# Performance work log

Hardware: AMD Instinct MI355X
Metric: run time of the kernel (lower is better)

The kernel has to match this reference:

```python
import jax, jax.numpy as jnp
import numpy as np

B, CIN, COUT, WID, M1, M2, H, W = 8, 3, 3, 16, 8, 8, 256, 256


def _fftfreq(n, d):
    # torch.fft.fftfreq(n, d); d may be a traced scalar
    k = np.concatenate([np.arange(0, (n - 1) // 2 + 1), np.arange(-(n // 2), 0)]).astype(np.float32)
    return jnp.asarray(k) / (n * d)


def _cplx(ri):
    return jax.lax.complex(ri[..., 0], ri[..., 1])


def _inorm(v, eps=1e-5):
    # InstanceNorm2d, affine=False: normalize over spatial dims per (b, c)
    mu = jnp.mean(v, axis=(-2, -1), keepdims=True)
    var = jnp.var(v, axis=(-2, -1), keepdims=True)
    return (v - mu) * jax.lax.rsqrt(var + eps)


def setup_inputs() -> dict:
    key = jax.random.key(0)
    ks = jax.random.split(key, 13)
    scale = 1.0 / (WID * WID)
    u = lambda k, s: scale * (0.5 + 0.5 * jax.random.uniform(k, s, jnp.float32))
    return {
        "x": jax.random.normal(ks[0], (B, CIN, H, W), jnp.float32),
        "fc0_w": jax.random.normal(ks[1], (CIN + 2, WID), jnp.float32) * 0.1,
        "fc0_b": jax.random.normal(ks[2], (WID,), jnp.float32) * 0.01,
        "pole1_ri": u(ks[3], (WID, WID, M1, 2)),
        "pole2_ri": u(ks[4], (WID, WID, M2, 2)),
        "residue_ri": u(ks[5], (WID, WID, M1, M2, 2)),
        "w0_w": jax.random.normal(ks[6], (WID, WID), jnp.float32) * 0.1,
        "w0_b": jax.random.normal(ks[7], (WID,), jnp.float32) * 0.01,
        "fc1_w": jax.random.normal(ks[8], (WID, 128), jnp.float32) * 0.1,
        "fc1_b": jax.random.normal(ks[9], (128,), jnp.float32) * 0.01,
        "fc2_w": jax.random.normal(ks[10], (128, COUT), jnp.float32) * 0.1,
        "fc2_b": jax.random.normal(ks[11], (COUT,), jnp.float32) * 0.01,
        "tx": jnp.linspace(0.0, 1.0, W, dtype=jnp.float32).reshape(1, W),
        "ty": jnp.linspace(0.0, 1.0, H, dtype=jnp.float32).reshape(1, H),
    }


def _pr2d(v, p1, p2, res, tx, ty):
    # v: [b, i, h, w] real; p1:[i,k,m1], p2:[i,k,m2], res:[i,k,m1,m2] complex
    b, i, h, w = v.shape
    dty = ty[0, 1] - ty[0, 0]
    dtx = tx[0, 1] - tx[0, 0]
    alpha = jnp.fft.fft2(v)  # [b,i,h,w] complex64
    lam1 = (2j * jnp.pi) * _fftfreq(h, dty)  # [h]
    lam2 = (2j * jnp.pi) * _fftfreq(w, dtx)  # [w]
    A1 = 1.0 / (lam1[None, None, None, :] - p1[..., None])  # [i,k,p,h]
    A2 = 1.0 / (lam2[None, None, None, :] - p2[..., None])  # [i,k,q,w]
    # output_residue1[b,k,o,x] = sum_{i,p,q} alpha[b,i,o,x] res[i,k,p,q] A1[i,k,p,o] A2[i,k,q,x]
    T = jnp.einsum('ikpq,ikpo->ikqo', res, A1)
    G = jnp.einsum('ikqo,ikqx->ikox', T, A2)        # [i,k,h,w] pole-residue transfer kernel
    out1 = jnp.einsum('biox,ikox->bkox', alpha, G)
    x1 = jnp.fft.ifft2(out1).real
    # output_residue2[b,k,p,q] = sum_{i,o,x} alpha[b,i,o,x] res[i,k,p,q] A1[i,k,p,o] A2[i,k,q,x]
    S = jnp.einsum('biox,ikqx->bikoq', alpha, A2)
    Mt = jnp.einsum('bikoq,ikpo->bikpq', S, A1)
    out2 = jnp.einsum('bikpq,ikpq->bkpq', Mt, res)  # [b,k,m1,m2]
    # transient part: x2[n,i,z,x] = sum_{b,p,q} out2[n,b,p,q] exp(p1[b,i,p] ty[z]) exp(p2[b,i,q] tx[x])
    tyc = ty.reshape(-1).astype(p1.dtype)
    txc = tx.reshape(-1).astype(p2.dtype)
    E1 = jnp.exp(p1[..., None] * tyc)  # [i,k,p,h]
    E2 = jnp.exp(p2[..., None] * txc)  # [i,k,q,w]
    U = jnp.einsum('nbpq,bipz->nbiqz', out2, E1)
    x2 = jnp.einsum('nbiqz,biqx->nizx', U, E2).real / (w * h)
    return x1 + x2


def reference(x, fc0_w, fc0_b, pole1_ri, pole2_ri, residue_ri, w0_w, w0_b,
              fc1_w, fc1_b, fc2_w, fc2_b, tx, ty):
    b, c, h, w = x.shape
    v = jnp.transpose(x, (0, 2, 3, 1))  # [b,h,w,c]
    gx = jnp.broadcast_to(jnp.linspace(0.0, 1.0, h, dtype=x.dtype)[None, :, None, None], (b, h, w, 1))
    gy = jnp.broadcast_to(jnp.linspace(0.0, 1.0, w, dtype=x.dtype)[None, None, :, None], (b, h, w, 1))
    v = jnp.concatenate([v, gx, gy], axis=-1)
    v = v @ fc0_w + fc0_b                 # [b,h,w,width]
    v = jnp.transpose(v, (0, 3, 1, 2))    # [b,width,h,w]
    p1, p2, res = _cplx(pole1_ri), _cplx(pole2_ri), _cplx(residue_ri)
    x1 = _inorm(_pr2d(_inorm(v), p1, p2, res, tx, ty))
    x2 = jnp.einsum('bihw,oi->bohw', v, w0_w) + w0_b[None, :, None, None]  # 1x1 conv
    u = x1 + x2
    u = jnp.transpose(u, (0, 2, 3, 1))
    u = jnp.sin(u @ fc1_w + fc1_b)
    u = u @ fc2_w + fc2_b
    return jnp.transpose(u, (0, 3, 1, 2))
```

## Files before the change

### kernel.cpp

```cpp
#include <hip/hip_runtime.h>
#include <cstddef>

#define NPIX 65536
#define PI_F 3.14159265358979323846f

__device__ __forceinline__ void cacc(float2& acc, float2 a, float2 b) {
  acc.x = fmaf(a.x, b.x, fmaf(-a.y, b.y, acc.x));
  acc.y = fmaf(a.x, b.y, fmaf(a.y, b.x, acc.y));
}

__device__ __forceinline__ void fft256_wave(float* re, float* im,
    const float* twr, const float* twi, int lane) {
  #pragma unroll
  for (int s = 0; s < 8; ++s) {
    __builtin_amdgcn_wave_barrier();
    const int half = 1 << s;
    #pragma unroll
    for (int r = 0; r < 2; ++r) {
      int m  = lane + 64*r;
      int t  = m & (half - 1);
      int g  = m >> s;
      int i0 = (g << (s+1)) + t;
      int i1 = i0 + half;
      int ti = t << (7 - s);
      float wr = twr[ti], wi = twi[ti];
      float br = re[i1], bi = im[i1];
      float vr = br*wr - bi*wi;
      float vi = br*wi + bi*wr;
      float ar = re[i0], ai = im[i0];
      re[i0] = ar + vr; im[i0] = ai + vi;
      re[i1] = ar - vr; im[i1] = ai - vi;
    }
  }
  __builtin_amdgcn_wave_barrier();
}

__global__ __launch_bounds__(256) void k_setup(const float2* __restrict__ p1,
    const float2* __restrict__ p2, const float* __restrict__ txv,
    const float* __restrict__ tyv, float2* __restrict__ A1,
    float2* __restrict__ A2T, float2* __restrict__ A2L,
    float2* __restrict__ E1, float2* __restrict__ E2) {
  int gid = blockIdx.x*256 + threadIdx.x;
  int o = gid & 255, p = (gid>>8)&7, k = (gid>>11)&15, i = gid>>15;
  float ko = (o < 128) ? (float)o : (float)(o - 256);
  float dty = tyv[1] - tyv[0];
  float dtx = txv[1] - txv[0];
  const float TWO_PI = 6.283185307179586f;
  {
    float lam = TWO_PI * ko / (256.0f * dty);
    float2 pv = p1[(i*16+k)*8 + p];
    float xr = -pv.x, yi = lam - pv.y;
    float D = xr*xr + yi*yi;
    A1[((size_t)((i*16+k)*8 + p))*256 + o] = make_float2(xr/D, -yi/D);
    float tv = tyv[o];
    float m = expf(pv.x*tv);
    E1[((size_t)((i*16+k)*8 + p))*256 + o] = make_float2(m*cosf(pv.y*tv), m*sinf(pv.y*tv));
  }
  {
    float lam = TWO_PI * ko / (256.0f * dtx);
    float2 pv = p2[(i*16+k)*8 + p];
    float xr = -pv.x, yi = lam - pv.y;
    float D = xr*xr + yi*yi;
    float2 val = make_float2(xr/D, -yi/D);
    A2T[((size_t)i*256 + o)*128 + k*8 + p] = val;
    A2L[((size_t)((i*16+k)*8 + p))*256 + o] = val;
    float tv = txv[o];
    float m = expf(pv.x*tv);
    E2[((size_t)((i*16+k)*8 + p))*256 + o] = make_float2(m*cosf(pv.y*tv), m*sinf(pv.y*tv));
  }
}

__global__ __launch_bounds__(256) void k_T(const float2* __restrict__ res,
    const float2* __restrict__ A1, float2* __restrict__ Tt) {
  int ik = blockIdx.x, tid = threadIdx.x;
  __shared__ float2 rbuf[64];
  __shared__ float2 a1[8][256];
  if (tid < 64) rbuf[tid] = res[(size_t)ik*64 + tid];
  for (int e = 0; e < 8; ++e) {
    int lin = tid + 256*e;
    int p = lin >> 8, o = lin & 255;
    a1[p][o] = A1[((size_t)ik*8 + p)*256 + o];
  }
  __syncthreads();
  int o = tid;
  #pragma unroll
  for (int q = 0; q < 8; ++q) {
    float2 acc = make_float2(0.f, 0.f);
    #pragma unroll
    for (int p = 0; p < 8; ++p) cacc(acc, rbuf[p*8+q], a1[p][o]);
    Tt[((size_t)ik*8 + q)*256 + o] = acc;
  }
}

__global__ __launch_bounds__(256) void k_stats_v(const float* __restrict__ x,
    const float* __restrict__ fc0w, const float* __restrict__ fc0b,
    float2* __restrict__ stats) {
  int img = blockIdx.x, tid = threadIdx.x;
  int k = img & 15, b = img >> 4;
  float w0 = fc0w[k], w1 = fc0w[16+k], w2 = fc0w[32+k], w3 = fc0w[48+k], w4 = fc0w[64+k];
  float base = fc0b[k] + (tid*(1.0f/255.0f))*w4;
  const float* xb = x + (size_t)b*3*NPIX;
  float s = 0.f, s2 = 0.f;
  for (int it = 0; it < 256; ++it) {
    int p = it*256 + tid;
    float val = base + (it*(1.0f/255.0f))*w3 + xb[p]*w0 + xb[NPIX+p]*w1 + xb[2*NPIX+p]*w2;
    s += val; s2 += val*val;
  }
  __shared__ float rs[256], rq[256];
  rs[tid] = s; rq[tid] = s2;
  __syncthreads();
  for (int off = 128; off > 0; off >>= 1) {
    if (tid < off) { rs[tid] += rs[tid+off]; rq[tid] += rq[tid+off]; }
    __syncthreads();
  }
  if (tid == 0) {
    float mean = rs[0] * (1.0f/65536.0f);
    float var  = rq[0] * (1.0f/65536.0f) - mean*mean;
    stats[img] = make_float2(mean, rsqrtf(var + 1e-5f));
  }
}

__global__ __launch_bounds__(256) void k_stats_p(const float* __restrict__ v,
    float2* __restrict__ stats) {
  int img = blockIdx.x, tid = threadIdx.x;
  const float* p = v + (size_t)img*NPIX;
  float s = 0.f, s2 = 0.f;
  for (int it = 0; it < 256; ++it) { float a = p[it*256 + tid]; s += a; s2 += a*a; }
  __shared__ float rs[256], rq[256];
  rs[tid] = s; rq[tid] = s2;
  __syncthreads();
  for (int off = 128; off > 0; off >>= 1) {
    if (tid < off) { rs[tid] += rs[tid+off]; rq[tid] += rq[tid+off]; }
    __syncthreads();
  }
  if (tid == 0) {
    float mean = rs[0] * (1.0f/65536.0f);
    float var  = rq[0] * (1.0f/65536.0f) - mean*mean;
    stats[img] = make_float2(mean, rsqrtf(var + 1e-5f));
  }
}

__global__ __launch_bounds__(256) void k_fft_v(const float* __restrict__ x,
    const float* __restrict__ fc0w, const float* __restrict__ fc0b,
    const float2* __restrict__ stats, float2* __restrict__ out) {
  __shared__ float sre[4][256], sim[4][256];
  __shared__ float twr[128], twi[128];
  int tid = threadIdx.x, lane = tid & 63, rowi = tid >> 6;
  int bid = blockIdx.x;
  int img = bid >> 6;
  int h   = (bid & 63)*4 + rowi;
  int k = img & 15, b = img >> 4;
  if (tid < 128) {
    float ang = (PI_F/128.0f)*tid;
    twr[tid] = cosf(ang); twi[tid] = -sinf(ang);
  }
  float2 st = stats[img];
  float w0 = fc0w[k], w1 = fc0w[16+k], w2 = fc0w[32+k], w3 = fc0w[48+k], w4 = fc0w[64+k];
  float bb = fc0b[k] + (h*(1.0f/255.0f))*w3;
  const float* xb = x + (size_t)b*3*NPIX + (size_t)h*256;
  float* re = sre[rowi]; float* im_ = sim[rowi];
  #pragma unroll
  for (int r = 0; r < 4; ++r) {
    int j = lane + 64*r;
    float val = bb + (j*(1.0f/255.0f))*w4 + xb[j]*w0 + xb[NPIX+j]*w1 + xb[2*NPIX+j]*w2;
    val = (val - st.x)*st.y;
    int bj = __brev((unsigned)j) >> 24;
    re[bj] = val; im_[bj] = 0.f;
  }
  __syncthreads();
  fft256_wave(re, im_, twr, twi, lane);
  float2* op = out + ((size_t)img*256 + h)*256;
  #pragma unroll
  for (int r = 0; r < 4; ++r) { int j = lane + 64*r; op[j] = make_float2(re[j], im_[j]); }
}

__global__ __launch_bounds__(256) void k_fft_colR(const float2* __restrict__ in,
    float2* __restrict__ outp) {
  __shared__ float tr[256][17], tim[256][17];
  __shared__ float twr[128], twi[128];
  int tid = threadIdx.x;
  int c = tid & 15, g = tid >> 4;
  int img = blockIdx.x >> 4;
  int c0  = (blockIdx.x & 15) * 16;
  if (tid < 128) {
    float ang = (PI_F/128.0f)*tid;
    twr[tid] = cosf(ang); twi[tid] = -sinf(ang);
  }
  const float2* base = in + (size_t)img*NPIX + c0;
  #pragma unroll
  for (int it = 0; it < 16; ++it) {
    int row = it*16 + g;
    float2 v = base[(size_t)row*256 + c];
    int br = __brev((unsigned)row) >> 24;
    tr[br][c] = v.x; tim[br][c] = v.y;
  }
  __syncthreads();
  int lane = tid & 63, w = tid >> 6;
  int cw = w*4 + (lane >> 4);
  int gw = lane & 15;
  for (int s = 0; s < 8; ++s) {
    __builtin_amdgcn_wave_barrier();
    int half = 1 << s;
    #pragma unroll
    for (int r = 0; r < 8; ++r) {
      int m  = gw + 16*r;
      int t  = m & (half - 1);
      int grp = m >> s;
      int i0 = (grp << (s+1)) + t;
      int i1 = i0 + half;
      int twx = t << (7 - s);
      float wr = twr[twx], wi = twi[twx];
      float br = tr[i1][cw], bi = tim[i1][cw];
      float vr = br*wr - bi*wi, vi = br*wi + bi*wr;
      float ar = tr[i0][cw], ai = tim[i0][cw];
      tr[i0][cw] = ar + vr; tim[i0][cw] = ai + vi;
      tr[i1][cw] = ar - vr; tim[i1][cw] = ai - vi;
    }
  }
  __syncthreads();
  #pragma unroll
  for (int it = 0; it < 16; ++it) {
    int row = it*16 + g;
    outp[((size_t)row*128 + img)*256 + c0 + c] = make_float2(tr[row][c], tim[row][c]);
  }
}

__global__ __launch_bounds__(256) void k_ifft_col_real(const float2* __restrict__ in,
    float* __restrict__ outp, float scale) {
  __shared__ float tr[256][17], tim[256][17];
  __shared__ float twr[128], twi[128];
  int tid = threadIdx.x;
  int c = tid & 15, g = tid >> 4;
  int img = blockIdx.x >> 4;
  int c0  = (blockIdx.x & 15) * 16;
  if (tid < 128) {
    float ang = (PI_F/128.0f)*tid;
    twr[tid] = cosf(ang); twi[tid] = sinf(ang);
  }
  const float2* base = in + (size_t)img*NPIX + c0;
  #pragma unroll
  for (int it = 0; it < 16; ++it) {
    int row = it*16 + g;
    float2 v = base[(size_t)row*256 + c];
    int br = __brev((unsigned)row) >> 24;
    tr[br][c] = v.x; tim[br][c] = v.y;
  }
  __syncthreads();
  int lane = tid & 63, w = tid >> 6;
  int cw = w*4 + (lane >> 4);
  int gw = lane & 15;
  for (int s = 0; s < 8; ++s) {
    __builtin_amdgcn_wave_barrier();
    int half = 1 << s;
    #pragma unroll
    for (int r = 0; r < 8; ++r) {
      int m  = gw + 16*r;
      int t  = m & (half - 1);
      int grp = m >> s;
      int i0 = (grp << (s+1)) + t;
      int i1 = i0 + half;
      int twx = t << (7 - s);
      float wr = twr[twx], wi = twi[twx];
      float br = tr[i1][cw], bi = tim[i1][cw];
      float vr = br*wr - bi*wi, vi = br*wi + bi*wr;
      float ar = tr[i0][cw], ai = tim[i0][cw];
      tr[i0][cw] = ar + vr; tim[i0][cw] = ai + vi;
      tr[i1][cw] = ar - vr; tim[i1][cw] = ai - vi;
    }
  }
  __syncthreads();
  float* ob = outp + (size_t)img*NPIX + c0;
  #pragma unroll
  for (int it = 0; it < 16; ++it) {
    int row = it*16 + g;
    ob[(size_t)row*256 + c] = tr[row][c]*scale;
  }
}

__global__ __launch_bounds__(256) void k_S(const float2* __restrict__ alphaR,
    const float2* __restrict__ A2T, float2* __restrict__ S) {
  __shared__ float2 al[16][256];
  int bid = blockIdx.x;
  int oblk = bid & 15, ni = bid >> 4;
  int i = ni & 15;
  int tid = threadIdx.x;
  for (int r = 0; r < 16; ++r)
    al[r][tid] = alphaR[((size_t)(oblk*16 + r)*128 + ni)*256 + tid];
  __syncthreads();
  int j = tid & 127, oh = tid >> 7;
  float2 acc[8];
  #pragma unroll
  for (int ol = 0; ol < 8; ++ol) acc[ol] = make_float2(0.f, 0.f);
  const float2* a2p = A2T + (size_t)i*32768 + j;
  float2 p0 = a2p[0], p1 = a2p[128], p2 = a2p[256], p3 = a2p[384];
  for (int xx = 0; xx < 256; xx += 4) {
    float2 a0 = p0, a1 = p1, a2v = p2, a3 = p3;
    int nx = xx + 4;
    if (nx < 256) {
      p0 = a2p[(size_t)nx*128];       p1 = a2p[(size_t)(nx+1)*128];
      p2 = a2p[(size_t)(nx+2)*128];   p3 = a2p[(size_t)(nx+3)*128];
    }
    #pragma unroll
    for (int ol = 0; ol < 8; ++ol) {
      cacc(acc[ol], al[oh*8+ol][xx],   a0);
      cacc(acc[ol], al[oh*8+ol][xx+1], a1);
      cacc(acc[ol], al[oh*8+ol][xx+2], a2v);
      cacc(acc[ol], al[oh*8+ol][xx+3], a3);
    }
  }
  #pragma unroll
  for (int ol = 0; ol < 8; ++ol) {
    int o = oblk*16 + oh*8 + ol;
    S[((size_t)ni*256 + o)*128 + j] = acc[ol];
  }
}

__global__ __launch_bounds__(256) void k_Mt(const float2* __restrict__ S,
    const float2* __restrict__ A1, float2* __restrict__ Mt) {
  __shared__ float2 sl[8][258];
  __shared__ float2 a1l[8][258];
  __shared__ float2 part[4][64];
  int bid = blockIdx.x;
  int k = bid & 15, ni = bid >> 4;
  int i = ni & 15;
  int ik = i*16 + k;
  int tid = threadIdx.x;
  for (int e = 0; e < 8; ++e) {
    int lin = tid + 256*e;
    int o = lin >> 3, q = lin & 7;
    sl[q][o] = S[((size_t)ni*256 + o)*128 + k*8 + q];
  }
  for (int e = 0; e < 8; ++e) {
    int lin = tid + 256*e;
    int p = lin >> 8, o = lin & 255;
    a1l[p][o] = A1[((size_t)ik*8 + p)*256 + o];
  }
  __syncthreads();
  int oq = tid >> 6, pq = tid & 63, p = pq >> 3, q = pq & 7;
  float2 acc = make_float2(0.f, 0.f);
  int o0 = oq*64;
  for (int o = o0; o < o0 + 64; ++o) cacc(acc, sl[q][o], a1l[p][o]);
  part[oq][pq] = acc;
  __syncthreads();
  if (oq == 0) {
    float2 a = part[0][pq], b = part[1][pq], c = part[2][pq], d = part[3][pq];
    acc.x = a.x + b.x + c.x + d.x;
    acc.y = a.y + b.y + c.y + d.y;
    Mt[(size_t)bid*64 + pq] = acc;
  }
}

__global__ __launch_bounds__(256) void k_out2(const float2* __restrict__ Mt,
    const float2* __restrict__ res, float2* __restrict__ out2) {
  int gid = blockIdx.x*256 + threadIdx.x;
  int pq = gid & 63, k = (gid >> 6) & 15, n = gid >> 10;
  float2 acc = make_float2(0.f, 0.f);
  for (int i = 0; i < 16; ++i)
    cacc(acc, Mt[((size_t)((n*16+i)*16 + k))*64 + pq], res[((size_t)(i*16+k))*64 + pq]);
  out2[((size_t)(n*16+k))*64 + pq] = acc;
}

__global__ __launch_bounds__(256) void k_out1g(const float2* __restrict__ alphaR,
    const float2* __restrict__ Tt, const float2* __restrict__ A2L,
    float2* __restrict__ out1) {
  __shared__ float2 tl[2][128];
  __shared__ float sre[4][256], sim[4][256];
  __shared__ float twr[128], twi[128];
  int d = blockIdx.x;
  int xcd = d & 7, idx = d >> 3;
  int o  = xcd*32 + (idx >> 3);
  int kh = idx & 7;
  int tid = threadIdx.x, x = tid;
  int lane = tid & 63, rowi = tid >> 6;
  {
    int kk = tid >> 7, rem = tid & 127;
    int i = rem >> 3, q = rem & 7;
    tl[kk][rem] = Tt[((size_t)((i*16 + 2*kh + kk)*8 + q))*256 + o];
  }
  if (tid < 128) {
    float ang = (PI_F/128.0f)*tid;
    twr[tid] = cosf(ang); twi[tid] = sinf(ang);
  }
  __syncthreads();
  float2 g0[16], g1[16];
  #pragma unroll
  for (int i = 0; i < 16; ++i) {
    const float2* a2k0 = &A2L[((size_t)((i*16 + 2*kh + 0)*8))*256 + x];
    const float2* a2k1 = &A2L[((size_t)((i*16 + 2*kh + 1)*8))*256 + x];
    float2 acc0 = make_float2(0.f, 0.f), acc1 = make_float2(0.f, 0.f);
    #pragma unroll
    for (int q = 0; q < 8; ++q) {
      cacc(acc0, tl[0][i*8+q], a2k0[(size_t)q*256]);
      cacc(acc1, tl[1][i*8+q], a2k1[(size_t)q*256]);
    }
    g0[i] = acc0; g1[i] = acc1;
  }
  const float2* arow = alphaR + (size_t)o*128*256 + x;
  int bj = __brev((unsigned)x) >> 24;
  for (int bp = 0; bp < 4; ++bp) {
    #pragma unroll
    for (int bb = 0; bb < 2; ++bb) {
      int b = bp*2 + bb;
      float2 acc0 = make_float2(0.f, 0.f), acc1 = make_float2(0.f, 0.f);
      #pragma unroll
      for (int i = 0; i < 16; ++i) {
        float2 al = arow[(size_t)(b*16 + i)*256];
        cacc(acc0, al, g0[i]);
        cacc(acc1, al, g1[i]);
      }
      sre[bb*2+0][bj] = acc0.x; sim[bb*2+0][bj] = acc0.y;
      sre[bb*2+1][bj] = acc1.x; sim[bb*2+1][bj] = acc1.y;
    }
    __syncthreads();
    fft256_wave(sre[rowi], sim[rowi], twr, twi, lane);
    int img = (bp*2 + (rowi >> 1))*16 + 2*kh + (rowi & 1);
    float2* op = out1 + ((size_t)img*256 + o)*256;
    #pragma unroll
    for (int r = 0; r < 4; ++r) {
      int jj = lane + 64*r;
      op[jj] = make_float2(sre[rowi][jj], sim[rowi][jj]);
    }
    __syncthreads();
  }
}

__global__ __launch_bounds__(256) void k_x2t(const float2* __restrict__ out2,
    const float2* __restrict__ E1, const float2* __restrict__ E2,
    float* __restrict__ x1pre) {
  int bid = blockIdx.x;
  int zb = bid & 31, nk = bid >> 5;
  int kk = nk & 15, n = nk >> 4;
  int x = threadIdx.x;
  __shared__ float2 o2[1024];
  __shared__ float2 e1l[1024];
  __shared__ float2 ul[1024];
  for (int e = 0; e < 4; ++e) {
    int lin = threadIdx.x + 256*e;
    int j = lin >> 6, pq = lin & 63;
    o2[lin] = out2[((size_t)(n*16 + j))*64 + pq];
  }
  for (int e = 0; e < 4; ++e) {
    int lin = threadIdx.x + 256*e;
    int j = lin >> 6, p = (lin >> 3) & 7, zz = lin & 7;
    e1l[lin] = E1[(((size_t)(j*16 + kk))*8 + p)*256 + zb*8 + zz];
  }
  __syncthreads();
  for (int e = 0; e < 4; ++e) {
    int lin = threadIdx.x + 256*e;
    int j = lin >> 6, q = (lin >> 3) & 7, zz = lin & 7;
    float2 acc = make_float2(0.f, 0.f);
    #pragma unroll
    for (int p = 0; p < 8; ++p) cacc(acc, o2[j*64 + p*8 + q], e1l[j*64 + p*8 + zz]);
    ul[lin] = acc;
  }
  __syncthreads();
  float acc[8] = {0.f,0.f,0.f,0.f,0.f,0.f,0.f,0.f};
  const float2* e2b = E2 + (size_t)kk*2048 + x;
  float2 nxt = e2b[0];
  for (int jq = 0; jq < 128; ++jq) {
    float2 e2 = nxt;
    int njq = jq + 1;
    if (njq < 128) {
      int nj = njq >> 3, nq = njq & 7;
      nxt = e2b[(size_t)nj*32768 + (size_t)nq*256];
    }
    const float4* up4 = reinterpret_cast<const float4*>(&ul[jq*8]);
    float4 u01 = up4[0], u23 = up4[1], u45 = up4[2], u67 = up4[3];
    acc[0] = fmaf(u01.x, e2.x, fmaf(-u01.y, e2.y, acc[0]));
    acc[1] = fmaf(u01.z, e2.x, fmaf(-u01.w, e2.y, acc[1]));
    acc[2] = fmaf(u23.x, e2.x, fmaf(-u23.y, e2.y, acc[2]));
    acc[3] = fmaf(u23.z, e2.x, fmaf(-u23.w, e2.y, acc[3]));
    acc[4] = fmaf(u45.x, e2.x, fmaf(-u45.y, e2.y, acc[4]));
    acc[5] = fmaf(u45.z, e2.x, fmaf(-u45.w, e2.y, acc[5]));
    acc[6] = fmaf(u67.x, e2.x, fmaf(-u67.y, e2.y, acc[6]));
    acc[7] = fmaf(u67.z, e2.x, fmaf(-u67.w, e2.y, acc[7]));
  }
  const float sc = 1.0f/65536.0f;
  #pragma unroll
  for (int zz = 0; zz < 8; ++zz) {
    size_t idx = (((size_t)nk)*256 + zb*8 + zz)*256 + x;
    x1pre[idx] += acc[zz]*sc;
  }
}

__global__ __launch_bounds__(256) void k_final(const float* __restrict__ x,
    const float* __restrict__ x1pre, const float2* __restrict__ stats2,
    const float* __restrict__ fc0w, const float* __restrict__ fc0b,
    const float* __restrict__ w0w, const float* __restrict__ w0b,
    const float* __restrict__ fc1w, const float* __restrict__ fc1b,
    const float* __restrict__ fc2w, const float* __restrict__ fc2b,
    float* __restrict__ out) {
  __shared__ float s_fc1w[2048], s_fc1b[128], s_fc2w[384], s_w0w[256], s_w0b[16], s_fc2b[3];
  int tid = threadIdx.x;
  for (int e = 0; e < 8; ++e) s_fc1w[tid + 256*e] = fc1w[tid + 256*e];
  if (tid < 128) s_fc1b[tid] = fc1b[tid];
  for (int e = 0; e < 2; ++e) { int q = tid + 256*e; if (q < 384) s_fc2w[q] = fc2w[q]; }
  s_w0w[tid] = w0w[tid];
  if (tid < 16) s_w0b[tid] = w0b[tid];
  if (tid < 3)  s_fc2b[tid] = fc2b[tid];
  __syncthreads();

  int bid = blockIdx.x;
  int hh = bid & 255, b = bid >> 8;
  int ww = tid;
  size_t pix = (size_t)hh*256 + ww;
  float xc0 = x[((size_t)b*3 + 0)*NPIX + pix];
  float xc1 = x[((size_t)b*3 + 1)*NPIX + pix];
  float xc2 = x[((size_t)b*3 + 2)*NPIX + pix];
  float gx = hh*(1.0f/255.0f), gy = ww*(1.0f/255.0f);
  float v[16], x1n[16], uo[16];
  #pragma unroll
  for (int k = 0; k < 16; ++k)
    v[k] = fc0b[k] + xc0*fc0w[k] + xc1*fc0w[16+k] + xc2*fc0w[32+k] + gx*fc0w[48+k] + gy*fc0w[64+k];
  #pragma unroll
  for (int k = 0; k < 16; ++k) {
    float2 st = stats2[b*16 + k];
    float xv = x1pre[((size_t)(b*16 + k))*NPIX + pix];
    x1n[k] = (xv - st.x)*st.y;
  }
  #pragma unroll
  for (int o = 0; o < 16; ++o) {
    float acc = s_w0b[o];
    #pragma unroll
    for (int k = 0; k < 16; ++k) acc = fmaf(v[k], s_w0w[o*16+k], acc);
    uo[o] = acc + x1n[o];
  }
  float o0 = 0.f, o1 = 0.f, o2 = 0.f;
  for (int jj = 0; jj < 128; ++jj) {
    float t = s_fc1b[jj];
    #pragma unroll
    for (int k = 0; k < 16; ++k) t = fmaf(uo[k], s_fc1w[k*128 + jj], t);
    float s = __sinf(t);
    o0 = fmaf(s, s_fc2w[jj*3+0], o0);
    o1 = fmaf(s, s_fc2w[jj*3+1], o1);
    o2 = fmaf(s, s_fc2w[jj*3+2], o2);
  }
  out[((size_t)b*3 + 0)*NPIX + pix] = o0 + s_fc2b[0];
  out[((size_t)b*3 + 1)*NPIX + pix] = o1 + s_fc2b[1];
  out[((size_t)b*3 + 2)*NPIX + pix] = o2 + s_fc2b[2];
}

extern "C" void kernel_launch(void* const* d_in, const int* in_sizes, int n_in,
                              void* d_out, int out_size, void* d_ws, size_t ws_size,
                              hipStream_t stream) {
  const float*  x    = (const float*)d_in[0];
  const float*  fc0w = (const float*)d_in[1];
  const float*  fc0b = (const float*)d_in[2];
  const float2* p1   = (const float2*)d_in[3];
  const float2* p2   = (const float2*)d_in[4];
  const float2* res  = (const float2*)d_in[5];
  const float*  w0w  = (const float*)d_in[6];
  const float*  w0b  = (const float*)d_in[7];
  const float*  fc1w = (const float*)d_in[8];
  const float*  fc1b = (const float*)d_in[9];
  const float*  fc2w = (const float*)d_in[10];
  const float*  fc2b = (const float*)d_in[11];
  const float*  txv  = (const float*)d_in[12];
  const float*  tyv  = (const float*)d_in[13];
  float* out = (float*)d_out;

  const size_t OFF_A1   = 0;
  const size_t OFF_A2T  = 4194304;
  const size_t OFF_E1   = 8388608;
  const size_t OFF_E2   = 12582912;
  const size_t OFF_ST1  = 16777216;
  const size_t OFF_ST2  = 16778240;
  const size_t OFF_OUT2 = 16779264;
  const size_t OFF_MT   = 16844800;
  const size_t OFF_S    = 17893376;
  const size_t OFF_X1   = 51447808;
  const size_t OFF_A    = 85002240;
  const size_t OFF_B    = 152111104;
  const size_t OFF_G    = 219219968;
  const size_t NEED     = 252774400;
  if (ws_size < NEED) return;
  char* ws = (char*)d_ws;
  float2* A1  = (float2*)(ws + OFF_A1);
  float2* A2T = (float2*)(ws + OFF_A2T);
  float2* E1  = (float2*)(ws + OFF_E1);
  float2* E2  = (float2*)(ws + OFF_E2);
  float2* st1 = (float2*)(ws + OFF_ST1);
  float2* st2 = (float2*)(ws + OFF_ST2);
  float2* o2b = (float2*)(ws + OFF_OUT2);
  float2* Mt  = (float2*)(ws + OFF_MT);
  float2* Sb  = (float2*)(ws + OFF_S);
  float2* Tt  = (float2*)(ws + OFF_X1);
  float*  X1  = (float*)(ws + OFF_X1);
  float2* Ab  = (float2*)(ws + OFF_A);
  float2* Bb  = (float2*)(ws + OFF_B);
  float2* A2L = (float2*)(ws + OFF_G);

  k_setup  <<<2048, 256, 0, stream>>>(p1, p2, txv, tyv, A1, A2T, A2L, E1, E2);
  k_T      <<<256, 256, 0, stream>>>(res, A1, Tt);
  k_stats_v<<<128, 256, 0, stream>>>(x, fc0w, fc0b, st1);
  k_fft_v  <<<8192, 256, 0, stream>>>(x, fc0w, fc0b, st1, Ab);
  k_fft_colR<<<2048, 256, 0, stream>>>(Ab, Bb);
  k_S      <<<2048, 256, 0, stream>>>(Bb, A2T, Sb);
  k_Mt     <<<2048, 256, 0, stream>>>(Sb, A1, Mt);
  k_out2   <<<32, 256, 0, stream>>>(Mt, res, o2b);
  k_out1g  <<<2048, 256, 0, stream>>>(Bb, Tt, A2L, Ab);
  k_ifft_col_real<<<2048, 256, 0, stream>>>(Ab, X1, 1.0f/65536.0f);
  k_x2t    <<<4096, 256, 0, stream>>>(o2b, E1, E2, X1);
  k_stats_p<<<128, 256, 0, stream>>>(X1, st2);
  k_final  <<<2048, 256, 0, stream>>>(x, X1, st2, fc0w, fc0b,
                                      w0w, w0b, fc1w, fc1b, fc2w, fc2b, out);
}
```

Baseline: 617.9 us.

## Replace LDS-based radix-2 FFTs with register/shuffle FFTs in row kernels

```diff
diff --git a/kernel.cpp b/kernel.cpp
--- a/kernel.cpp
+++ b/kernel.cpp
@@ -8,31 +8,35 @@
   acc.x = fmaf(a.x, b.x, fmaf(-a.y, b.y, acc.x));
   acc.y = fmaf(a.x, b.y, fmaf(a.y, b.x, acc.y));
 }
-
-__device__ __forceinline__ void fft256_wave(float* re, float* im,
-    const float* twr, const float* twi, int lane) {
-  #pragma unroll
-  for (int s = 0; s < 8; ++s) {
-    __builtin_amdgcn_wave_barrier();
-    const int half = 1 << s;
-    #pragma unroll
-    for (int r = 0; r < 2; ++r) {
-      int m  = lane + 64*r;
-      int t  = m & (half - 1);
-      int g  = m >> s;
-      int i0 = (g << (s+1)) + t;
-      int i1 = i0 + half;
-      int ti = t << (7 - s);
-      float wr = twr[ti], wi = twi[ti];
-      float br = re[i1], bi = im[i1];
-      float vr = br*wr - bi*wi;
-      float vi = br*wi + bi*wr;
-      float ar = re[i0], ai = im[i0];
-      re[i0] = ar + vr; im[i0] = ai + vi;
-      re[i1] = ar - vr; im[i1] = ai - vi;
-    }
-  }
-  __builtin_amdgcn_wave_barrier();
+__device__ __forceinline__ float2 cmulf(float2 a, float2 b) {
+  return make_float2(a.x*b.x - a.y*b.y, a.x*b.y + a.y*b.x);
+}
+__device__ __forceinline__ float2 add2(float2 a, float2 b) { return make_float2(a.x+b.x, a.y+b.y); }
+__device__ __forceinline__ float2 sub2(float2 a, float2 b) { return make_float2(a.x-b.x, a.y-b.y); }
+__device__ __forceinline__ float2 shflc(float2 v, int mask) {
+  return make_float2(__shfl_xor(v.x, mask), __shfl_xor(v.y, mask));
+}
+__device__ __forceinline__ void make_tw(float sgn, int l, float2* tw) {
+  const float c = sgn * (2.0f*PI_F/256.0f);
+  int idxs[8] = { l, 64+l, 2*l, (l&31)<<2, (l&15)<<3, (l&7)<<4, (l&3)<<5, (l&1)<<6 };
+  #pragma unroll
+  for (int r = 0; r < 8; ++r) { float sn, cs; __sincosf(c*idxs[r], &sn, &cs); tw[r] = make_float2(cs, sn); }
+}
+__device__ __forceinline__ void fwd_stage(float2& vv, int lane, int H, float2 tws, bool unit) {
+  float2 p = shflc(vv, H);
+  bool up = (lane & H) != 0;
+  float2 lo = add2(vv, p);
+  float2 df = sub2(p, vv);
+  float2 hi = unit ? df : cmulf(df, tws);
+  vv = up ? hi : lo;
+}
+__device__ __forceinline__ void inv_stage(float2& vv, int lane, int H, float2 tws, bool unit) {
+  float2 p = shflc(vv, H);
+  bool up = (lane & H) != 0;
+  float2 bv = up ? vv : p;
+  float2 av = up ? p : vv;
+  float2 t = unit ? bv : cmulf(bv, tws);
+  vv = up ? sub2(av, t) : add2(av, t);
 }
 
 __global__ __launch_bounds__(256) void k_setup(const float2* __restrict__ p1,
@@ -57,7 +61,9 @@
     E1[((size_t)((i*16+k)*8 + p))*256 + o] = make_float2(m*cosf(pv.y*tv), m*sinf(pv.y*tv));
   }
   {
-    float lam = TWO_PI * ko / (256.0f * dtx);
+    int fo = __brev((unsigned)o) >> 24;
+    float ko2 = (fo < 128) ? (float)fo : (float)(fo - 256);
+    float lam = TWO_PI * ko2 / (256.0f * dtx);
     float2 pv = p2[(i*16+k)*8 + p];
     float xr = -pv.x, yi = lam - pv.y;
     float D = xr*xr + yi*yi;
@@ -143,35 +149,48 @@
 __global__ __launch_bounds__(256) void k_fft_v(const float* __restrict__ x,
     const float* __restrict__ fc0w, const float* __restrict__ fc0b,
     const float2* __restrict__ stats, float2* __restrict__ out) {
-  __shared__ float sre[4][256], sim[4][256];
-  __shared__ float twr[128], twi[128];
   int tid = threadIdx.x, lane = tid & 63, rowi = tid >> 6;
   int bid = blockIdx.x;
   int img = bid >> 6;
   int h   = (bid & 63)*4 + rowi;
   int k = img & 15, b = img >> 4;
-  if (tid < 128) {
-    float ang = (PI_F/128.0f)*tid;
-    twr[tid] = cosf(ang); twi[tid] = -sinf(ang);
-  }
   float2 st = stats[img];
   float w0 = fc0w[k], w1 = fc0w[16+k], w2 = fc0w[32+k], w3 = fc0w[48+k], w4 = fc0w[64+k];
   float bb = fc0b[k] + (h*(1.0f/255.0f))*w3;
   const float* xb = x + (size_t)b*3*NPIX + (size_t)h*256;
-  float* re = sre[rowi]; float* im_ = sim[rowi];
-  #pragma unroll
-  for (int r = 0; r < 4; ++r) {
-    int j = lane + 64*r;
-    float val = bb + (j*(1.0f/255.0f))*w4 + xb[j]*w0 + xb[NPIX+j]*w1 + xb[2*NPIX+j]*w2;
-    val = (val - st.x)*st.y;
-    int bj = __brev((unsigned)j) >> 24;
-    re[bj] = val; im_[bj] = 0.f;
-  }
-  __syncthreads();
-  fft256_wave(re, im_, twr, twi, lane);
+  float2 tw[8];
+  make_tw(-1.0f, lane, tw);
+  float2 v0, v1, v2, v3;
+  {
+    #pragma unroll
+    for (int e = 0; e < 4; ++e) {
+      int j = e*64 + lane;
+      float val = bb + (j*(1.0f/255.0f))*w4 + xb[j]*w0 + xb[NPIX+j]*w1 + xb[2*NPIX+j]*w2;
+      val = (val - st.x)*st.y;
+      float2 c = make_float2(val, 0.f);
+      if (e == 0) v0 = c; else if (e == 1) v1 = c; else if (e == 2) v2 = c; else v3 = c;
+    }
+  }
+  { float2 n0 = add2(v0, v2), n2 = cmulf(sub2(v0, v2), tw[0]);
+    float2 n1 = add2(v1, v3), n3 = cmulf(sub2(v1, v3), tw[1]);
+    v0 = n0; v1 = n1; v2 = n2; v3 = n3; }
+  { float2 n0 = add2(v0, v1), n1 = cmulf(sub2(v0, v1), tw[2]);
+    float2 n2 = add2(v2, v3), n3 = cmulf(sub2(v2, v3), tw[2]);
+    v0 = n0; v1 = n1; v2 = n2; v3 = n3; }
+  fwd_stage(v0, lane, 32, tw[3], false); fwd_stage(v1, lane, 32, tw[3], false);
+  fwd_stage(v2, lane, 32, tw[3], false); fwd_stage(v3, lane, 32, tw[3], false);
+  fwd_stage(v0, lane, 16, tw[4], false); fwd_stage(v1, lane, 16, tw[4], false);
+  fwd_stage(v2, lane, 16, tw[4], false); fwd_stage(v3, lane, 16, tw[4], false);
+  fwd_stage(v0, lane,  8, tw[5], false); fwd_stage(v1, lane,  8, tw[5], false);
+  fwd_stage(v2, lane,  8, tw[5], false); fwd_stage(v3, lane,  8, tw[5], false);
+  fwd_stage(v0, lane,  4, tw[6], false); fwd_stage(v1, lane,  4, tw[6], false);
+  fwd_stage(v2, lane,  4, tw[6], false); fwd_stage(v3, lane,  4, tw[6], false);
+  fwd_stage(v0, lane,  2, tw[7], false); fwd_stage(v1, lane,  2, tw[7], false);
+  fwd_stage(v2, lane,  2, tw[7], false); fwd_stage(v3, lane,  2, tw[7], false);
+  fwd_stage(v0, lane,  1, tw[0], true ); fwd_stage(v1, lane,  1, tw[0], true );
+  fwd_stage(v2, lane,  1, tw[0], true ); fwd_stage(v3, lane,  1, tw[0], true );
   float2* op = out + ((size_t)img*256 + h)*256;
-  #pragma unroll
-  for (int r = 0; r < 4; ++r) { int j = lane + 64*r; op[j] = make_float2(re[j], im_[j]); }
+  op[lane] = v0; op[64+lane] = v1; op[128+lane] = v2; op[192+lane] = v3;
 }
 
 __global__ __launch_bounds__(256) void k_fft_colR(const float2* __restrict__ in,
@@ -360,67 +379,65 @@
   out2[((size_t)(n*16+k))*64 + pq] = acc;
 }
 
-__global__ __launch_bounds__(256) void k_out1g(const float2* __restrict__ alphaR,
+__global__ __launch_bounds__(256) void k_out1w(const float2* __restrict__ alphaR,
     const float2* __restrict__ Tt, const float2* __restrict__ A2L,
     float2* __restrict__ out1) {
-  __shared__ float2 tl[2][128];
-  __shared__ float sre[4][256], sim[4][256];
-  __shared__ float twr[128], twi[128];
+  __shared__ float2 tl[128];
+  __shared__ float2 gl[16][256];
   int d = blockIdx.x;
   int xcd = d & 7, idx = d >> 3;
-  int o  = xcd*32 + (idx >> 3);
-  int kh = idx & 7;
-  int tid = threadIdx.x, x = tid;
-  int lane = tid & 63, rowi = tid >> 6;
-  {
-    int kk = tid >> 7, rem = tid & 127;
-    int i = rem >> 3, q = rem & 7;
-    tl[kk][rem] = Tt[((size_t)((i*16 + 2*kh + kk)*8 + q))*256 + o];
-  }
+  int o = xcd*32 + (idx >> 4);
+  int k = idx & 15;
+  int tid = threadIdx.x, x = tid, lane = tid & 63, w = tid >> 6;
   if (tid < 128) {
-    float ang = (PI_F/128.0f)*tid;
-    twr[tid] = cosf(ang); twi[tid] = sinf(ang);
-  }
-  __syncthreads();
-  float2 g0[16], g1[16];
+    int i = tid >> 3, q = tid & 7;
+    tl[tid] = Tt[((size_t)((i*16 + k)*8 + q))*256 + o];
+  }
+  float2 tw[8];
+  make_tw(+1.0f, lane, tw);
+  __syncthreads();
   #pragma unroll
   for (int i = 0; i < 16; ++i) {
-    const float2* a2k0 = &A2L[((size_t)((i*16 + 2*kh + 0)*8))*256 + x];
-    const float2* a2k1 = &A2L[((size_t)((i*16 + 2*kh + 1)*8))*256 + x];
-    float2 acc0 = make_float2(0.f, 0.f), acc1 = make_float2(0.f, 0.f);
-    #pragma unroll
-    for (int q = 0; q < 8; ++q) {
-      cacc(acc0, tl[0][i*8+q], a2k0[(size_t)q*256]);
-      cacc(acc1, tl[1][i*8+q], a2k1[(size_t)q*256]);
+    const float2* a2 = &A2L[((size_t)((i*16 + k)*8))*256 + x];
+    float2 acc = make_float2(0.f, 0.f);
+    #pragma unroll
+    for (int q = 0; q < 8; ++q) cacc(acc, tl[i*8+q], a2[(size_t)q*256]);
+    gl[i][x] = acc;
+  }
+  __syncthreads();
+  const float2* abase = alphaR + (size_t)o*128*256;
+  for (int bi = 0; bi < 2; ++bi) {
+    int b = w + bi*4;
+    float2 v0 = make_float2(0.f,0.f), v1 = v0, v2 = v0, v3 = v0;
+    #pragma unroll
+    for (int i = 0; i < 16; ++i) {
+      const float2* ar = abase + (size_t)(b*16 + i)*256;
+      float2 a0 = ar[lane], a1 = ar[64+lane], a2v = ar[128+lane], a3 = ar[192+lane];
+      cacc(v0, a0,  gl[i][lane]);
+      cacc(v1, a1,  gl[i][64+lane]);
+      cacc(v2, a2v, gl[i][128+lane]);
+      cacc(v3, a3,  gl[i][192+lane]);
     }
-    g0[i] = acc0; g1[i] = acc1;
-  }
-  const float2* arow = alphaR + (size_t)o*128*256 + x;
-  int bj = __brev((unsigned)x) >> 24;
-  for (int bp = 0; bp < 4; ++bp) {
-    #pragma unroll
-    for (int bb = 0; bb < 2; ++bb) {
-      int b = bp*2 + bb;
-      float2 acc0 = make_float2(0.f, 0.f), acc1 = make_float2(0.f, 0.f);
-      #pragma unroll
-      for (int i = 0; i < 16; ++i) {
-        float2 al = arow[(size_t)(b*16 + i)*256];
-        cacc(acc0, al, g0[i]);
-        cacc(acc1, al, g1[i]);
-      }
-      sre[bb*2+0][bj] = acc0.x; sim[bb*2+0][bj] = acc0.y;
-      sre[bb*2+1][bj] = acc1.x; sim[bb*2+1][bj] = acc1.y;
-    }
-    __syncthreads();
-    fft256_wave(sre[rowi], sim[rowi], twr, twi, lane);
-    int img = (bp*2 + (rowi >> 1))*16 + 2*kh + (rowi & 1);
-    float2* op = out1 + ((size_t)img*256 + o)*256;
-    #pragma unroll
-    for (int r = 0; r < 4; ++r) {
-      int jj = lane + 64*r;
-      op[jj] = make_float2(sre[rowi][jj], sim[rowi][jj]);
-    }
-    __syncthreads();
+    inv_stage(v0, lane, 1, tw[0], true ); inv_stage(v1, lane, 1, tw[0], true );
+    inv_stage(v2, lane, 1, tw[0], true ); inv_stage(v3, lane, 1, tw[0], true );
+    inv_stage(v0, lane, 2, tw[7], false); inv_stage(v1, lane, 2, tw[7], false);
+    inv_stage(v2, lane, 2, tw[7], false); inv_stage(v3, lane, 2, tw[7], false);
+    inv_stage(v0, lane, 4, tw[6], false); inv_stage(v1, lane, 4, tw[6], false);
+    inv_stage(v2, lane, 4, tw[6], false); inv_stage(v3, lane, 4, tw[6], false);
+    inv_stage(v0, lane, 8, tw[5], false); inv_stage(v1, lane, 8, tw[5], false);
+    inv_stage(v2, lane, 8, tw[5], false); inv_stage(v3, lane, 8, tw[5], false);
+    inv_stage(v0, lane, 16, tw[4], false); inv_stage(v1, lane, 16, tw[4], false);
+    inv_stage(v2, lane, 16, tw[4], false); inv_stage(v3, lane, 16, tw[4], false);
+    inv_stage(v0, lane, 32, tw[3], false); inv_stage(v1, lane, 32, tw[3], false);
+    inv_stage(v2, lane, 32, tw[3], false); inv_stage(v3, lane, 32, tw[3], false);
+    { float2 t01 = cmulf(v1, tw[2]); float2 n0 = add2(v0, t01), n1 = sub2(v0, t01);
+      float2 t23 = cmulf(v3, tw[2]); float2 n2 = add2(v2, t23), n3 = sub2(v2, t23);
+      v0 = n0; v1 = n1; v2 = n2; v3 = n3; }
+    { float2 t02 = cmulf(v2, tw[0]); float2 n0 = add2(v0, t02), n2 = sub2(v0, t02);
+      float2 t13 = cmulf(v3, tw[1]); float2 n1 = add2(v1, t13), n3 = sub2(v1, t13);
+      v0 = n0; v2 = n2; v1 = n1; v3 = n3; }
+    float2* op = out1 + ((size_t)(b*16 + k)*256 + o)*256;
+    op[lane] = v0; op[64+lane] = v1; op[128+lane] = v2; op[192+lane] = v3;
   }
 }
 
@@ -598,7 +615,7 @@
   k_S      <<<2048, 256, 0, stream>>>(Bb, A2T, Sb);
   k_Mt     <<<2048, 256, 0, stream>>>(Sb, A1, Mt);
   k_out2   <<<32, 256, 0, stream>>>(Mt, res, o2b);
-  k_out1g  <<<2048, 256, 0, stream>>>(Bb, Tt, A2L, Ab);
+  k_out1w  <<<4096, 256, 0, stream>>>(Bb, Tt, A2L, Ab);
   k_ifft_col_real<<<2048, 256, 0, stream>>>(Ab, X1, 1.0f/65536.0f);
   k_x2t    <<<4096, 256, 0, stream>>>(o2b, E1, E2, X1);
   k_stats_p<<<128, 256, 0, stream>>>(X1, st2);
```

Measured after the change: 629.9 us. No clear change (+1.9%).
